# Kernel tuning notes

Hardware: AMD Instinct MI355X
Metric: run time of the kernel (lower is better)

Reference implementation:

```python
import jax, jax.numpy as jnp
import numpy as np


def setup_inputs() -> dict:
    key = jax.random.key(0)
    k1, k2, k3 = jax.random.split(key, 3)
    # N, C, H, W per input_specs
    x = jax.random.normal(k1, (16, 8, 1024, 1024), dtype=jnp.float32)
    # weight: (out_channels, in_channels, kH, kW)
    weight = jax.random.normal(k2, (8, 8, 3, 3), dtype=jnp.float32) * 0.1
    bias = jax.random.normal(k3, (8,), dtype=jnp.float32) * 0.1
    return {"x": x, "weight": weight, "bias": bias}


def reference(x, weight, bias):
    # DietConv2dV2's tiled per-kernel-column matmul loop is mathematically a
    # standard direct conv2d (stride=1, padding=1) followed by a bias add.
    out = jax.lax.conv_general_dilated(
        x, weight,
        window_strides=(1, 1),
        padding=((1, 1), (1, 1)),
        dimension_numbers=("NCHW", "OIHW", "NCHW"),
    )
    return out + bias[None, :, None, None]
```

## Files before the change

### kernel.cpp

```cpp
#include <hip/hip_runtime.h>


#define R 4
#define HH 1024
#define WW 1024
#define CI 8
#define CO 8

__global__ __launch_bounds__(256) void conv3x3_kernel(
    const float* __restrict__ x,
    const float* __restrict__ wgt,
    const float* __restrict__ bias,
    float* __restrict__ out)
{
    const int w  = blockIdx.x * 256 + threadIdx.x;
    const int h0 = blockIdx.y * R;
    const int n  = blockIdx.z;

    const long HW = (long)HH * WW;
    const float* xn = x + (long)n * CI * HW;

    float acc[CO][R];
#pragma unroll
    for (int co = 0; co < CO; ++co) {
        const float b = bias[co];
#pragma unroll
        for (int r = 0; r < R; ++r) acc[co][r] = b;
    }

    for (int ci = 0; ci < CI; ++ci) {
        const float* xc = xn + (long)ci * HW;

        float in[R + 2][3];
#pragma unroll
        for (int r = 0; r < R + 2; ++r) {
            const int h = h0 - 1 + r;
            const bool hv = (h >= 0) && (h < HH);
            const float* row = xc + (long)h * WW;
#pragma unroll
            for (int c = 0; c < 3; ++c) {
                const int wc = w - 1 + c;
                const bool v = hv && (wc >= 0) && (wc < WW);
                in[r][c] = v ? row[wc] : 0.0f;
            }
        }

#pragma unroll
        for (int co = 0; co < CO; ++co) {
            const float* wp = wgt + ((co * CI + ci) * 9);
            float wv[9];
#pragma unroll
            for (int k = 0; k < 9; ++k) wv[k] = wp[k];
#pragma unroll
            for (int r = 0; r < R; ++r) {
#pragma unroll
                for (int kh = 0; kh < 3; ++kh) {
#pragma unroll
                    for (int kw = 0; kw < 3; ++kw) {
                        acc[co][r] = fmaf(in[r + kh][kw], wv[kh * 3 + kw], acc[co][r]);
                    }
                }
            }
        }
    }

#pragma unroll
    for (int co = 0; co < CO; ++co) {
        float* op = out + ((long)n * CO + co) * HW + (long)h0 * WW + w;
#pragma unroll
        for (int r = 0; r < R; ++r) {
            op[(long)r * WW] = acc[co][r];
        }
    }
}

extern "C" void kernel_launch(void* const* d_in, const int* in_sizes, int n_in,
                              void* d_out, int out_size, void* d_ws, size_t ws_size,
                              hipStream_t stream) {
    const float* x    = (const float*)d_in[0];
    const float* wgt  = (const float*)d_in[1];
    const float* bias = (const float*)d_in[2];
    float* out = (float*)d_out;

    dim3 grid(WW / 256, HH / R, 16);
    dim3 block(256, 1, 1);
    conv3x3_kernel<<<grid, block, 0, stream>>>(x, wgt, bias, out);
}
```

Baseline: 322.5 us.

## Compute four horizontal outputs per thread with float4 loads and stores

Each thread now covers four adjacent output columns and two rows instead of one column and four rows. Inputs are read as float4 plus two halo scalars, and outputs are written as float4. One block spans a full 1024-wide row, so the grid is rearranged. This cuts redundant horizontal input loads and the number of memory instructions. The cost is more register pressure (64 accumulators) and more vertical halo rereads with R=2.

```diff
diff --git a/kernel.cpp b/kernel.cpp
--- a/kernel.cpp
+++ b/kernel.cpp
@@ -1,7 +1,7 @@
 #include <hip/hip_runtime.h>
 
 
-#define R 4
+#define R 2
 #define HH 1024
 #define WW 1024
 #define CI 8
@@ -13,36 +13,45 @@
     const float* __restrict__ bias,
     float* __restrict__ out)
 {
-    const int w  = blockIdx.x * 256 + threadIdx.x;
-    const int h0 = blockIdx.y * R;
-    const int n  = blockIdx.z;
+    const int w0 = threadIdx.x * 4;
+    const int h0 = blockIdx.x * R;
+    const int n  = blockIdx.y;
 
     const long HW = (long)HH * WW;
     const float* xn = x + (long)n * CI * HW;
 
-    float acc[CO][R];
+    float acc[CO][R][4];
 #pragma unroll
     for (int co = 0; co < CO; ++co) {
         const float b = bias[co];
 #pragma unroll
-        for (int r = 0; r < R; ++r) acc[co][r] = b;
+        for (int r = 0; r < R; ++r)
+#pragma unroll
+            for (int p = 0; p < 4; ++p) acc[co][r][p] = b;
     }
 
     for (int ci = 0; ci < CI; ++ci) {
         const float* xc = xn + (long)ci * HW;
 
-        float in[R + 2][3];
+        float in[R + 2][6];
 #pragma unroll
         for (int r = 0; r < R + 2; ++r) {
             const int h = h0 - 1 + r;
             const bool hv = (h >= 0) && (h < HH);
             const float* row = xc + (long)h * WW;
-#pragma unroll
-            for (int c = 0; c < 3; ++c) {
-                const int wc = w - 1 + c;
-                const bool v = hv && (wc >= 0) && (wc < WW);
-                in[r][c] = v ? row[wc] : 0.0f;
+            float4 mid;
+            float left, right;
+            if (hv) {
+                mid   = *reinterpret_cast<const float4*>(row + w0);
+                left  = (w0 > 0)        ? row[w0 - 1] : 0.0f;
+                right = (w0 + 4 < WW)   ? row[w0 + 4] : 0.0f;
+            } else {
+                mid = make_float4(0.f, 0.f, 0.f, 0.f);
+                left = 0.f; right = 0.f;
             }
+            in[r][0] = left;
+            in[r][1] = mid.x; in[r][2] = mid.y; in[r][3] = mid.z; in[r][4] = mid.w;
+            in[r][5] = right;
         }
 
 #pragma unroll
@@ -52,24 +61,26 @@
 #pragma unroll
             for (int k = 0; k < 9; ++k) wv[k] = wp[k];
 #pragma unroll
-            for (int r = 0; r < R; ++r) {
+            for (int r = 0; r < R; ++r)
 #pragma unroll
-                for (int kh = 0; kh < 3; ++kh) {
+                for (int kh = 0; kh < 3; ++kh)
 #pragma unroll
-                    for (int kw = 0; kw < 3; ++kw) {
-                        acc[co][r] = fmaf(in[r + kh][kw], wv[kh * 3 + kw], acc[co][r]);
-                    }
-                }
-            }
+                    for (int kw = 0; kw < 3; ++kw)
+#pragma unroll
+                        for (int p = 0; p < 4; ++p)
+                            acc[co][r][p] = fmaf(in[r + kh][p + kw], wv[kh * 3 + kw],
+                                                 acc[co][r][p]);
         }
     }
 
 #pragma unroll
     for (int co = 0; co < CO; ++co) {
-        float* op = out + ((long)n * CO + co) * HW + (long)h0 * WW + w;
+        float* op = out + ((long)n * CO + co) * HW + (long)h0 * WW + w0;
 #pragma unroll
         for (int r = 0; r < R; ++r) {
-            op[(long)r * WW] = acc[co][r];
+            float4 v = make_float4(acc[co][r][0], acc[co][r][1],
+                                   acc[co][r][2], acc[co][r][3]);
+            *reinterpret_cast<float4*>(op + (long)r * WW) = v;
         }
     }
 }
@@ -82,7 +93,7 @@
     const float* bias = (const float*)d_in[2];
     float* out = (float*)d_out;
 
-    dim3 grid(WW / 256, HH / R, 16);
+    dim3 grid(HH / R, 16, 1);
     dim3 block(256, 1, 1);
     conv3x3_kernel<<<grid, block, 0, stream>>>(x, wgt, bias, out);
 }
```

Result: slower. 350.8 us (+8.8%).

## Use packed FP32 FMA over row pairs with duplicated weights

Applied to the files above, without the earlier changes.

Replaces scalar FMAs with v_pk_fma_f32 that computes two output rows at once, using weights pre-duplicated into float2 pairs by a small setup kernel in the workspace. Rows per thread drop from four to two, so the vertical input halo overhead increases. Aims to halve FMA instruction count in a compute-heavy conv, at the cost of more input reads, an extra launch, and reliance on inline asm with scalar-operand constraints.

```diff
diff --git a/kernel.cpp b/kernel.cpp
--- a/kernel.cpp
+++ b/kernel.cpp
@@ -1,39 +1,49 @@
 #include <hip/hip_runtime.h>
 
 
-#define R 4
+typedef __attribute__((ext_vector_type(2))) float f32x2;
+
 #define HH 1024
 #define WW 1024
 #define CI 8
 #define CO 8
 
-__global__ __launch_bounds__(256) void conv3x3_kernel(
+__global__ void dup_weights_kernel(const float* __restrict__ wgt,
+                                   f32x2* __restrict__ dup) {
+    const int i = threadIdx.x;
+    if (i < CO * CI * 9) {
+        const float w = wgt[i];
+        f32x2 p; p.x = w; p.y = w;
+        dup[i] = p;
+    }
+}
+
+__global__ __launch_bounds__(256) void conv3x3_pk_kernel(
     const float* __restrict__ x,
-    const float* __restrict__ wgt,
+    const f32x2* __restrict__ wdup,
     const float* __restrict__ bias,
     float* __restrict__ out)
 {
     const int w  = blockIdx.x * 256 + threadIdx.x;
-    const int h0 = blockIdx.y * R;
+    const int h0 = blockIdx.y * 2;
     const int n  = blockIdx.z;
 
     const long HW = (long)HH * WW;
     const float* xn = x + (long)n * CI * HW;
 
-    float acc[CO][R];
+    f32x2 acc[CO];
 #pragma unroll
     for (int co = 0; co < CO; ++co) {
         const float b = bias[co];
-#pragma unroll
-        for (int r = 0; r < R; ++r) acc[co][r] = b;
+        acc[co].x = b; acc[co].y = b;
     }
 
     for (int ci = 0; ci < CI; ++ci) {
         const float* xc = xn + (long)ci * HW;
 
-        float in[R + 2][3];
+        float in[4][3];
 #pragma unroll
-        for (int r = 0; r < R + 2; ++r) {
+        for (int r = 0; r < 4; ++r) {
             const int h = h0 - 1 + r;
             const bool hv = (h >= 0) && (h < HH);
             const float* row = xc + (long)h * WW;
@@ -45,32 +55,35 @@
             }
         }
 
+        f32x2 pk[3][3];
+#pragma unroll
+        for (int kh = 0; kh < 3; ++kh)
+#pragma unroll
+            for (int c = 0; c < 3; ++c) {
+                pk[kh][c].x = in[kh][c];
+                pk[kh][c].y = in[kh + 1][c];
+            }
+
 #pragma unroll
         for (int co = 0; co < CO; ++co) {
-            const float* wp = wgt + ((co * CI + ci) * 9);
-            float wv[9];
+            const f32x2* wp = wdup + ((co * CI + ci) * 9);
 #pragma unroll
-            for (int k = 0; k < 9; ++k) wv[k] = wp[k];
+            for (int kh = 0; kh < 3; ++kh)
 #pragma unroll
-            for (int r = 0; r < R; ++r) {
-#pragma unroll
-                for (int kh = 0; kh < 3; ++kh) {
-#pragma unroll
-                    for (int kw = 0; kw < 3; ++kw) {
-                        acc[co][r] = fmaf(in[r + kh][kw], wv[kh * 3 + kw], acc[co][r]);
-                    }
+                for (int kw = 0; kw < 3; ++kw) {
+                    const f32x2 w2 = wp[kh * 3 + kw];
+                    asm("v_pk_fma_f32 %0, %1, %2, %0"
+                        : "+v"(acc[co])
+                        : "v"(pk[kh][kw]), "s"(w2));
                 }
-            }
         }
     }
 
 #pragma unroll
     for (int co = 0; co < CO; ++co) {
         float* op = out + ((long)n * CO + co) * HW + (long)h0 * WW + w;
-#pragma unroll
-        for (int r = 0; r < R; ++r) {
-            op[(long)r * WW] = acc[co][r];
-        }
+        op[0]  = acc[co].x;
+        op[WW] = acc[co].y;
     }
 }
 
@@ -81,8 +94,11 @@
     const float* wgt  = (const float*)d_in[1];
     const float* bias = (const float*)d_in[2];
     float* out = (float*)d_out;
+    f32x2* wdup = (f32x2*)d_ws;
 
-    dim3 grid(WW / 256, HH / R, 16);
+    dup_weights_kernel<<<1, 576, 0, stream>>>(wgt, wdup);
+
+    dim3 grid(WW / 256, HH / 2, 16);
     dim3 block(256, 1, 1);
-    conv3x3_kernel<<<grid, block, 0, stream>>>(x, wgt, bias, out);
+    conv3x3_pk_kernel<<<grid, block, 0, stream>>>(x, wdup, bias, out);
 }
```

Measured after the change: 351.0 us. +8.8%, slower.

## Stage input tiles in double-buffered LDS with register prefetch of next channel

Applied to the files above, without the earlier changes.

Each block now loads its input rows plus left and right halo columns for one channel into shared memory and reads the 3x3 neighbourhoods from there. Previously each thread issued three overlapping global loads per row. The next channel is prefetched into registers while the current one is computed, then written to the alternate LDS buffer, so global latency overlaps with FMAs. This costs a barrier per channel, extra registers and LDS use that may lower occupancy. Redundant neighbour loads were mostly served by L1/L2 already in a memory-bound kernel.

```diff
diff --git a/kernel.cpp b/kernel.cpp
--- a/kernel.cpp
+++ b/kernel.cpp
@@ -1,49 +1,89 @@
 #include <hip/hip_runtime.h>
 
 
-#define R 4
 #define HH 1024
 #define WW 1024
 #define CI 8
 #define CO 8
+#define RT 4
+#define LW 258
 
-__global__ __launch_bounds__(256) void conv3x3_kernel(
+__global__ __launch_bounds__(256) void conv3x3_lds_kernel(
     const float* __restrict__ x,
     const float* __restrict__ wgt,
     const float* __restrict__ bias,
     float* __restrict__ out)
 {
-    const int w  = blockIdx.x * 256 + threadIdx.x;
-    const int h0 = blockIdx.y * R;
-    const int n  = blockIdx.z;
+    __shared__ float lds[2][RT + 2][LW];
+
+    const int tid = threadIdx.x;
+    const int w0  = blockIdx.x * 256;
+    const int w   = w0 + tid;
+    const int h0  = blockIdx.y * RT;
+    const int n   = blockIdx.z;
 
     const long HW = (long)HH * WW;
     const float* xn = x + (long)n * CI * HW;
 
-    float acc[CO][R];
+    const bool halo  = (tid < 12);
+    const int  hrow  = (tid < 6) ? tid : (tid - 6);
+    const int  hcol  = (tid < 6) ? (w0 - 1) : (w0 + 256);
+    const int  hlcol = (tid < 6) ? 0 : (LW - 1);
+    const bool hcok  = (hcol >= 0) && (hcol < WW);
+
+    float acc[CO][RT];
 #pragma unroll
     for (int co = 0; co < CO; ++co) {
         const float b = bias[co];
 #pragma unroll
-        for (int r = 0; r < R; ++r) acc[co][r] = b;
+        for (int r = 0; r < RT; ++r) acc[co][r] = b;
     }
 
+    {
+        const float* xc = xn;
+#pragma unroll
+        for (int r = 0; r < RT + 2; ++r) {
+            const int h = h0 - 1 + r;
+            float v = 0.0f;
+            if (h >= 0 && h < HH) v = xc[(long)h * WW + w];
+            lds[0][r][tid + 1] = v;
+        }
+        if (halo) {
+            const int h = h0 - 1 + hrow;
+            float v = 0.0f;
+            if (hcok && h >= 0 && h < HH) v = xc[(long)h * WW + hcol];
+            lds[0][hrow][hlcol] = v;
+        }
+    }
+    __syncthreads();
+
     for (int ci = 0; ci < CI; ++ci) {
-        const float* xc = xn + (long)ci * HW;
+        const int buf = ci & 1;
 
-        float in[R + 2][3];
+        float ld[RT + 2];
+        float ldh = 0.0f;
+        if (ci < CI - 1) {
+            const float* xc = xn + (long)(ci + 1) * HW;
 #pragma unroll
-        for (int r = 0; r < R + 2; ++r) {
-            const int h = h0 - 1 + r;
-            const bool hv = (h >= 0) && (h < HH);
-            const float* row = xc + (long)h * WW;
-#pragma unroll
-            for (int c = 0; c < 3; ++c) {
-                const int wc = w - 1 + c;
-                const bool v = hv && (wc >= 0) && (wc < WW);
-                in[r][c] = v ? row[wc] : 0.0f;
+            for (int r = 0; r < RT + 2; ++r) {
+                const int h = h0 - 1 + r;
+                float v = 0.0f;
+                if (h >= 0 && h < HH) v = xc[(long)h * WW + w];
+                ld[r] = v;
+            }
+            if (halo) {
+                const int h = h0 - 1 + hrow;
+                if (hcok && h >= 0 && h < HH) ldh = xc[(long)h * WW + hcol];
             }
         }
+
+        const float* lp = &lds[buf][0][tid];
+        float in[RT + 2][3];
+#pragma unroll
+        for (int r = 0; r < RT + 2; ++r)
+#pragma unroll
+            for (int c = 0; c < 3; ++c)
+                in[r][c] = lp[r * LW + c];
 
 #pragma unroll
         for (int co = 0; co < CO; ++co) {
@@ -52,25 +92,30 @@
 #pragma unroll
             for (int k = 0; k < 9; ++k) wv[k] = wp[k];
 #pragma unroll
-            for (int r = 0; r < R; ++r) {
+            for (int r = 0; r < RT; ++r)
 #pragma unroll
-                for (int kh = 0; kh < 3; ++kh) {
+                for (int kh = 0; kh < 3; ++kh)
 #pragma unroll
-                    for (int kw = 0; kw < 3; ++kw) {
-                        acc[co][r] = fmaf(in[r + kh][kw], wv[kh * 3 + kw], acc[co][r]);
-                    }
-                }
-            }
+                    for (int kw = 0; kw < 3; ++kw)
+                        acc[co][r] = fmaf(in[r + kh][kw], wv[kh * 3 + kw],
+                                          acc[co][r]);
         }
+
+        if (ci < CI - 1) {
+            const int nb = buf ^ 1;
+#pragma unroll
+            for (int r = 0; r < RT + 2; ++r) lds[nb][r][tid + 1] = ld[r];
+            if (halo) lds[nb][hrow][hlcol] = ldh;
+        }
+        __syncthreads();
     }
 
 #pragma unroll
     for (int co = 0; co < CO; ++co) {
         float* op = out + ((long)n * CO + co) * HW + (long)h0 * WW + w;
 #pragma unroll
-        for (int r = 0; r < R; ++r) {
+        for (int r = 0; r < RT; ++r)
             op[(long)r * WW] = acc[co][r];
-        }
     }
 }
 
@@ -82,7 +127,7 @@
     const float* bias = (const float*)d_in[2];
     float* out = (float*)d_out;
 
-    dim3 grid(WW / 256, HH / R, 16);
+    dim3 grid(WW / 256, HH / RT, 16);
     dim3 block(256, 1, 1);
-    conv3x3_kernel<<<grid, block, 0, stream>>>(x, wgt, bias, out);
+    conv3x3_lds_kernel<<<grid, block, 0, stream>>>(x, wgt, bias, out);
 }
```

Result: faster. 305.9 us (-5.2%).
